# Performance work log

Measured on AMD Instinct MI355X. Metric: run time of the kernel, lower is better.

## Reference

```python
import jax, jax.numpy as jnp
import numpy as np

H = 16       # num heads
D = 128      # head_dim
R = 64       # d_rope_latent
HID = 2048   # hidden_size
DL = 512     # d_latent
EPS = 1e-6


def _rmsnorm(x, g):
    return x * jax.lax.rsqrt(jnp.mean(x * x, axis=-1, keepdims=True) + EPS) * g


def setup_inputs() -> dict:
    key = jax.random.key(0)
    ks = jax.random.split(key, 8)
    B, S = 2, 2048
    s = 0.02
    return {
        "x":   jax.random.normal(ks[0], (B, S, HID), jnp.float32),
        "Wq":  jax.random.normal(ks[1], (HID, H * D), jnp.float32) * s,
        "Wkv": jax.random.normal(ks[2], (HID, DL), jnp.float32) * s,
        "Wkr": jax.random.normal(ks[3], (DL, H * R), jnp.float32) * s,
        "Wkn": jax.random.normal(ks[4], (DL, H * (D - R)), jnp.float32) * s,
        "Wv":  jax.random.normal(ks[5], (DL, H * D), jnp.float32) * s,
        "Wo":  jax.random.normal(ks[6], (H * D, HID), jnp.float32) * s,
        "gq":  jnp.ones((D,), jnp.float32),
        "gk":  jnp.ones((D,), jnp.float32),
    }


def reference(x, Wq, Wkv, Wkr, Wkn, Wv, Wo, gq, gk):
    B, S, _ = x.shape
    # q projection + per-head RMSNorm
    q = _rmsnorm((x @ Wq).reshape(B, S, H, D), gq)          # [B,S,H,D]
    # low-rank KV latent
    lat = x @ Wkv                                            # [B,S,DL]
    kr = (lat @ Wkr).reshape(B, S, H, R)                     # rope part
    kn = (lat @ Wkn).reshape(B, S, H, D - R)                 # nope part
    # pos_encoding is None in source -> no rotation applied, just concat
    k = _rmsnorm(jnp.concatenate([kr, kn], axis=-1), gk)     # [B,S,H,D]
    v = (lat @ Wv).reshape(B, S, H, D)
    # causal SDPA
    scale = 1.0 / jnp.sqrt(jnp.float32(D))
    scores = jnp.einsum('bqhd,bkhd->bhqk', q, k) * scale     # [B,H,S,S]
    causal = jnp.tril(jnp.ones((S, S), bool))
    scores = jnp.where(causal, scores, jnp.float32(-1e30))
    p = jax.nn.softmax(scores, axis=-1)
    o = jnp.einsum('bhqk,bkhd->bqhd', p, v).reshape(B, S, H * D)
    return o @ Wo
```

## Files before the change

kernel.cpp:

```cpp
#include <hip/hip_runtime.h>
#include <cstdint>
#include <cstddef>

typedef short v8s __attribute__((ext_vector_type(8)));
typedef float v4f __attribute__((ext_vector_type(4)));

__device__ inline float bs2f(short s) {
    return __uint_as_float(((unsigned int)(unsigned short)s) << 16);
}
__device__ inline short f2bs(float f) {
    unsigned int u = __float_as_uint(f);
    unsigned int r = (u + 0x7fffu + ((u >> 16) & 1u)) >> 16;
    return (short)r;
}

#define MFMA(a, b, c) __builtin_amdgcn_mfma_f32_16x16x32_bf16((a), (b), (c), 0, 0, 0)

#define GLOAD_LDS16(g, l)                                                  \
    __builtin_amdgcn_global_load_lds(                                      \
        (const __attribute__((address_space(1))) void*)(g),                \
        (__attribute__((address_space(3))) void*)(l), 16, 0, 0)

__global__ __launch_bounds__(256) void prep(const float* __restrict__ x,
                                            short* __restrict__ xb,
                                            const float* __restrict__ Wq,
                                            const float* __restrict__ Wkv,
                                            const float* __restrict__ Wkr,
                                            const float* __restrict__ Wkn,
                                            const float* __restrict__ Wv,
                                            const float* __restrict__ Wo,
                                            short* __restrict__ WtA,
                                            short* __restrict__ WtB,
                                            short* __restrict__ Wot) {
    int blk = blockIdx.x;
    if (blk < 8192) {
        int i = (blk * 256 + threadIdx.x) * 4;
        float4 v = *(const float4*)(x + i);
        short r[4] = {f2bs(v.x), f2bs(v.y), f2bs(v.z), f2bs(v.w)};
        *(uint2*)(xb + i) = *(const uint2*)r;
        return;
    }
    blk -= 8192;
    const float* W;
    short* Wt;
    int K, N, bx, by;
    if (blk < 4096)      { W = Wq;  Wt = WtA;                      K = 2048; N = 2048; bx = blk & 63; by = blk >> 6; }
    else if (blk < 5120) { blk -= 4096; W = Wkv; Wt = WtA + (size_t)2048 * 2048; K = 2048; N = 512;  bx = blk & 15; by = blk >> 4; }
    else if (blk < 5632) { blk -= 5120; W = Wkr; Wt = WtB;                       K = 512;  N = 1024; bx = blk & 31; by = blk >> 5; }
    else if (blk < 6144) { blk -= 5632; W = Wkn; Wt = WtB + (size_t)1024 * 512;  K = 512;  N = 1024; bx = blk & 31; by = blk >> 5; }
    else if (blk < 7168) { blk -= 6144; W = Wv;  Wt = WtB + (size_t)2048 * 512;  K = 512;  N = 2048; bx = blk & 63; by = blk >> 6; }
    else                 { blk -= 7168; W = Wo;  Wt = Wot;                       K = 2048; N = 2048; bx = blk & 63; by = blk >> 6; }

    __shared__ float tile[32][33];
    const int tx = threadIdx.x & 31, ty = threadIdx.x >> 5;
    const int n0 = bx * 32, k0 = by * 32;
#pragma unroll
    for (int i = 0; i < 32; i += 8) tile[ty + i][tx] = W[(size_t)(k0 + ty + i) * N + n0 + tx];
    __syncthreads();
#pragma unroll
    for (int i = 0; i < 32; i += 8)
        Wt[(size_t)(n0 + ty + i) * K + k0 + tx] = f2bs(tile[tx][ty + i]);
}

__global__ __launch_bounds__(256) void gemm_bt(const short* __restrict__ A,
                                               const short* __restrict__ Bt,
                                               void* __restrict__ C0,
                                               void* __restrict__ C1,
                                               void* __restrict__ C2,
                                               int M, int N, int K, int mode,
                                               const float* __restrict__ g,
                                               float scale) {
    __shared__ short As[128 * 32];
    __shared__ short Bs[128 * 32];
    const int tid = threadIdx.x;
    const int lane = tid & 63, wave = tid >> 6;
    const int l16 = lane & 15, quad = lane >> 4;
    const int wm = (wave >> 1) * 64, wn = (wave & 1) * 64;

    const int gx = gridDim.x;
    const int nwg = gx * gridDim.y;
    const int wg = blockIdx.y * gx + blockIdx.x;
    const int cpx = nwg >> 3;
    const int swz = (wg & 7) * cpx + (wg >> 3);
    const int m0 = (swz / gx) * 128, n0 = (swz % gx) * 128;

    const v4f VZ = {0.f, 0.f, 0.f, 0.f};
    v4f acc[4][4];
#pragma unroll
    for (int i = 0; i < 4; i++)
#pragma unroll
        for (int j = 0; j < 4; j++) acc[i][j] = VZ;

    const int r0 = wave * 32 + (lane >> 2);
    const int r1 = r0 + 16;
    const int c0 = ((lane & 3) ^ ((r0 >> 1) & 3)) * 8;
    const int c1 = ((lane & 3) ^ ((r1 >> 1) & 3)) * 8;
    const short* aSrc0 = A + (size_t)(m0 + r0) * K + c0;
    const short* aSrc1 = A + (size_t)(m0 + r1) * K + c1;
    const short* bSrc0 = Bt + (size_t)(n0 + r0) * K + c0;
    const short* bSrc1 = Bt + (size_t)(n0 + r1) * K + c1;
    short* const ldsA0 = &As[(wave * 32) * 32];
    short* const ldsA1 = &As[(wave * 32 + 16) * 32];
    short* const ldsB0 = &Bs[(wave * 32) * 32];
    short* const ldsB1 = &Bs[(wave * 32 + 16) * 32];

    for (int kk = 0; kk < K; kk += 32) {
        __syncthreads();
        GLOAD_LDS16(aSrc0 + kk, ldsA0);
        GLOAD_LDS16(aSrc1 + kk, ldsA1);
        GLOAD_LDS16(bSrc0 + kk, ldsB0);
        GLOAD_LDS16(bSrc1 + kk, ldsB1);
        __syncthreads();

        v8s af[4], bfr[4];
#pragma unroll
        for (int t = 0; t < 4; t++) {
            const int ra = wm + t * 16 + l16;
            af[t] = *(const v8s*)(&As[ra * 32 + ((quad ^ ((ra >> 1) & 3)) * 8)]);
        }
#pragma unroll
        for (int t = 0; t < 4; t++) {
            const int rb = wn + t * 16 + l16;
            bfr[t] = *(const v8s*)(&Bs[rb * 32 + ((quad ^ ((rb >> 1) & 3)) * 8)]);
        }
#pragma unroll
        for (int i = 0; i < 4; i++)
#pragma unroll
            for (int j = 0; j < 4; j++) acc[i][j] = MFMA(af[i], bfr[j], acc[i][j]);
    }

    if (mode == 2) {
        if (n0 < 2048) {
            __syncthreads();
            float* red = (float*)As;
#pragma unroll
            for (int i = 0; i < 4; i++) {
#pragma unroll
                for (int r = 0; r < 4; r++) {
                    float ss2 = 0.f;
#pragma unroll
                    for (int j = 0; j < 4; j++) { float v = acc[i][j][r]; ss2 += v * v; }
#pragma unroll
                    for (int off2 = 1; off2 < 16; off2 <<= 1) ss2 += __shfl_xor(ss2, off2);
                    if (l16 == 0) red[(wm + i * 16 + quad * 4 + r) * 2 + (wn >> 6)] = ss2;
                }
            }
            __syncthreads();
            float gv[4];
#pragma unroll
            for (int j = 0; j < 4; j++) gv[j] = g[wn + j * 16 + l16];
#pragma unroll
            for (int i = 0; i < 4; i++) {
#pragma unroll
                for (int r = 0; r < 4; r++) {
                    const int rl = wm + i * 16 + quad * 4 + r;
                    const float rs =
                        rsqrtf((red[rl * 2] + red[rl * 2 + 1]) * (1.f / 128.f) + 1e-6f) * scale;
#pragma unroll
                    for (int j = 0; j < 4; j++)
                        ((short*)C0)[(size_t)(m0 + rl) * 2048 + n0 + wn + j * 16 + l16] =
                            f2bs(acc[i][j][r] * rs * gv[j]);
                }
            }
        } else {
#pragma unroll
            for (int i = 0; i < 4; i++)
#pragma unroll
                for (int r = 0; r < 4; r++) {
                    const int row = m0 + wm + i * 16 + quad * 4 + r;
#pragma unroll
                    for (int j = 0; j < 4; j++)
                        ((short*)C1)[(size_t)row * 512 + n0 - 2048 + wn + j * 16 + l16] =
                            f2bs(acc[i][j][r]);
                }
        }
        return;
    }

    if (mode == 3 && n0 >= 2048) {
        short* C = (short*)C2;
#pragma unroll
        for (int i = 0; i < 4; i++) {
            const int row = m0 + wm + i * 16 + quad * 4;
            const int bq = row >> 11, s = row & 2047;
            const int kt = s >> 6, key = s & 63;
#pragma unroll
            for (int j = 0; j < 4; j++) {
                const int col = n0 - 2048 + wn + j * 16 + l16;
                const int hh = col >> 7, d = col & 127;
                size_t base = ((size_t)((bq * 16 + hh) * 32 + kt) * 128 + d) * 64 + key;
                short pk[4];
#pragma unroll
                for (int r = 0; r < 4; r++) pk[r] = f2bs(acc[i][j][r]);
                *(uint2*)(C + base) = *(const uint2*)pk;
            }
        }
        return;
    }

    void* Cb = C0;
    int ld = N, coff = 0;
    if (mode == 3) {
        if (n0 < 1024) { Cb = C0; ld = 1024; coff = 0; }
        else           { Cb = C1; ld = 1024; coff = 1024; }
    }
#pragma unroll
    for (int i = 0; i < 4; i++) {
#pragma unroll
        for (int r = 0; r < 4; r++) {
            const int row = m0 + wm + i * 16 + quad * 4 + r;
#pragma unroll
            for (int j = 0; j < 4; j++) {
                const int col = n0 - coff + wn + j * 16 + l16;
                float v = acc[i][j][r];
                if (mode == 1) ((float*)Cb)[(size_t)row * ld + col] = v;
                else ((short*)Cb)[(size_t)row * ld + col] = f2bs(v);
            }
        }
    }
}

__global__ __launch_bounds__(256) void rmsnorm_k(const short* __restrict__ KR,
                                                 const short* __restrict__ KN,
                                                 const float* __restrict__ g,
                                                 short* __restrict__ Y) {
    const int tid = threadIdx.x;
    const int rh = blockIdx.x * 32 + (tid >> 3);
    const int j = tid & 7;
    const size_t ibase = (size_t)blockIdx.x * 2048 + (size_t)tid * 8;
    v8s a = *(const v8s*)(KR + ibase);
    v8s c = *(const v8s*)(KN + ibase);
    float af[8], cf[8];
    float ss = 0.f;
#pragma unroll
    for (int t = 0; t < 8; t++) {
        af[t] = bs2f(a[t]);
        cf[t] = bs2f(c[t]);
        ss += af[t] * af[t] + cf[t] * cf[t];
    }
#pragma unroll
    for (int off = 1; off < 8; off <<= 1) ss += __shfl_xor(ss, off);
    const float rs = rsqrtf(ss * (1.f / 128.f) + 1e-6f);
    const int m = rh >> 4, h = rh & 15;
    const int b = m >> 11, s = m & 2047;
    const size_t obase = ((size_t)((b * 16 + h) * 32 + (s >> 6)) * 64 + (s & 63)) * 128;
    const float* gp = g + j * 8;
    v8s o0, o1;
#pragma unroll
    for (int t = 0; t < 8; t++) {
        o0[t] = f2bs(af[t] * rs * gp[t]);
        o1[t] = f2bs(cf[t] * rs * gp[64 + t]);
    }
    *(v8s*)(Y + obase + j * 8) = o0;
    *(v8s*)(Y + obase + 64 + j * 8) = o1;
}

#define PSTR 72

__global__ __launch_bounds__(256) void flash_attn(const short* __restrict__ Q,
                                                  const short* __restrict__ Kp,
                                                  const short* __restrict__ Vp,
                                                  short* __restrict__ O, int S) {
    __shared__ short Ks[64 * 128];
    __shared__ short Vs[128 * 64];
    __shared__ short Ps[4][16 * PSTR];

    const int lane = threadIdx.x & 63, w = threadIdx.x >> 6;
    const int l16 = lane & 15, quad = lane >> 4;
    const int blk = blockIdx.x;
    const int g = blk >> 3;
    const int bh = (blk & 7) * 4 + (g & 3);
    const int b = bh >> 4, h = bh & 15;
    const int qb = 31 - (g >> 2);
    const int q0 = qb * 64 + w * 16;

    const int koffE = (lane >> 4) * 128 + (((lane & 15) ^ (lane >> 4)) << 3);
    const int koffO = (lane >> 4) * 128 + (((lane & 15) ^ 4 ^ (lane >> 4)) << 3);
    const int voffc = (lane >> 3) * 64 + (((lane & 7) ^ (lane >> 3)) << 3);
    const int swz = (l16 & 7) * 8;

    v8s bq[4];
    {
        const size_t qbase = ((size_t)(b * S + q0 + l16) * 16 + h) * 128;
#pragma unroll
        for (int kc = 0; kc < 4; kc++)
            bq[kc] = *(const v8s*)(Q + qbase + kc * 32 + quad * 8);
    }

    const v4f VZ = {0.f, 0.f, 0.f, 0.f};
    v4f accO[8];
    v4f accL = VZ;
#pragma unroll
    for (int d = 0; d < 8; d++) accO[d] = VZ;

    const short o1 = 0x3F80;
    const v8s vones = {o1, o1, o1, o1, o1, o1, o1, o1};

    const short* const kbh = Kp + (size_t)(bh * 32) * 8192;
    const short* const vbh = Vp + (size_t)(bh * 32) * 8192;

    const int nkt = qb + 1;
    for (int kt = 0; kt < nkt; ++kt) {
        __syncthreads();
        {
            const short* kb = kbh + (size_t)kt * 8192;
            const short* vb = vbh + (size_t)kt * 8192;
            const int c0 = w * 4;
            GLOAD_LDS16(kb + (c0 + 0) * 512 + koffE, Ks + (c0 + 0) * 512);
            GLOAD_LDS16(kb + (c0 + 1) * 512 + koffO, Ks + (c0 + 1) * 512);
            GLOAD_LDS16(kb + (c0 + 2) * 512 + koffE, Ks + (c0 + 2) * 512);
            GLOAD_LDS16(kb + (c0 + 3) * 512 + koffO, Ks + (c0 + 3) * 512);
            GLOAD_LDS16(vb + (c0 + 0) * 512 + voffc, Vs + (c0 + 0) * 512);
            GLOAD_LDS16(vb + (c0 + 1) * 512 + voffc, Vs + (c0 + 1) * 512);
            GLOAD_LDS16(vb + (c0 + 2) * 512 + voffc, Vs + (c0 + 2) * 512);
            GLOAD_LDS16(vb + (c0 + 3) * 512 + voffc, Vs + (c0 + 3) * 512);
        }
        __syncthreads();

        v4f sc[4];
#pragma unroll
        for (int nt = 0; nt < 4; nt++) {
            v8s ak[4];
            const int krow = (nt * 16 + l16) * 128;
#pragma unroll
            for (int kc = 0; kc < 4; kc++)
                ak[kc] = *(const v8s*)(Ks + krow + ((quad * 8 + kc * 32) ^ swz));
            v4f s = VZ;
#pragma unroll
            for (int kc = 0; kc < 4; kc++) s = MFMA(ak[kc], bq[kc], s);
            sc[nt] = s;
        }

        if (kt == nkt - 1) {
            const int qrow = q0 + l16;
            const int k0 = kt * 64;
#pragma unroll
            for (int nt = 0; nt < 4; nt++)
#pragma unroll
                for (int r = 0; r < 4; r++)
                    if (k0 + nt * 16 + quad * 4 + r > qrow) sc[nt][r] = -1e30f;
        }

#pragma unroll
        for (int nt = 0; nt < 4; nt++) {
            short pk[4];
#pragma unroll
            for (int r = 0; r < 4; r++) {
                float p = exp2f(sc[nt][r] - 20.f);
                pk[r] = (short)(__float_as_uint(p) >> 16);
            }
            *(uint2*)(&Ps[w][l16 * PSTR + nt * 16 + quad * 4]) = *(const uint2*)pk;
        }

        v8s ap[2];
#pragma unroll
        for (int kc2 = 0; kc2 < 2; kc2++)
            ap[kc2] = *(const v8s*)(&Ps[w][l16 * PSTR + kc2 * 32 + quad * 8]);
#pragma unroll
        for (int dt = 0; dt < 8; dt++) {
            const int vrow = (dt * 16 + l16) * 64;
#pragma unroll
            for (int kc2 = 0; kc2 < 2; kc2++) {
                v8s bv = *(const v8s*)(Vs + vrow + ((quad * 8 + kc2 * 32) ^ swz));
                accO[dt] = MFMA(ap[kc2], bv, accO[dt]);
            }
        }
#pragma unroll
        for (int kc2 = 0; kc2 < 2; kc2++) accL = MFMA(ap[kc2], vones, accL);
    }

#pragma unroll
    for (int r = 0; r < 4; r++) {
        const int rl = quad * 4 + r;
        const int qg = q0 + rl;
        const float inv = 1.f / accL[r];
        const size_t obase = ((size_t)(b * S + qg) * 16 + h) * 128;
#pragma unroll
        for (int dt = 0; dt < 8; dt++)
            O[obase + dt * 16 + l16] = f2bs(accO[dt][r] * inv);
    }
}

extern "C" void kernel_launch(void* const* d_in, const int* in_sizes, int n_in,
                              void* d_out, int out_size, void* d_ws, size_t ws_size,
                              hipStream_t stream) {
    (void)in_sizes; (void)n_in; (void)out_size; (void)ws_size;
    const float* x   = (const float*)d_in[0];
    const float* Wq  = (const float*)d_in[1];
    const float* Wkv = (const float*)d_in[2];
    const float* Wkr = (const float*)d_in[3];
    const float* Wkn = (const float*)d_in[4];
    const float* Wv  = (const float*)d_in[5];
    const float* Wo  = (const float*)d_in[6];
    const float* gq  = (const float*)d_in[7];
    const float* gk  = (const float*)d_in[8];

    const int B = 2, S = 2048, HID = 2048;
    const int M = B * S;

    char* ws = (char*)d_ws;
    size_t off = 0;
    auto alloc = [&](size_t bytes) {
        char* p = ws + off;
        off += (bytes + 255) & ~(size_t)255;
        return p;
    };
    short* xb   = (short*)alloc((size_t)M * HID * 2);
    short* WtA  = (short*)alloc((size_t)2560 * 2048 * 2);
    short* WtB  = (short*)alloc((size_t)4096 * 512 * 2);
    short* Wot  = (short*)alloc((size_t)2048 * 2048 * 2);
    short* qb   = (short*)alloc((size_t)M * 2048 * 2);
    short* lat  = (short*)alloc((size_t)M * 512 * 2);
    short* krr  = (short*)alloc((size_t)M * 1024 * 2);
    short* knr  = (short*)alloc((size_t)M * 1024 * 2);
    short* Kp   = (short*)alloc((size_t)M * 2048 * 2);
    short* Vp   = (short*)alloc((size_t)M * 2048 * 2);
    short* ob   = (short*)alloc((size_t)M * 2048 * 2);

    prep<<<19456, 256, 0, stream>>>(x, xb, Wq, Wkv, Wkr, Wkn, Wv, Wo, WtA, WtB, Wot);

    gemm_bt<<<dim3(2560 / 128, M / 128), 256, 0, stream>>>(
        xb, WtA, qb, lat, nullptr, M, 2560, 2048, 2, gq,
        0.08838834764831845f * 1.4426950408889634f);

    gemm_bt<<<dim3(4096 / 128, M / 128), 256, 0, stream>>>(
        lat, WtB, krr, knr, Vp, M, 4096, 512, 3, nullptr, 0.f);
    rmsnorm_k<<<(M * 16) / 32, 256, 0, stream>>>(krr, knr, gk, Kp);

    flash_attn<<<dim3(1024), 256, 0, stream>>>(qb, Kp, Vp, ob, S);

    gemm_bt<<<dim3(2048 / 128, M / 128), 256, 0, stream>>>(
        ob, Wot, d_out, nullptr, nullptr, M, 2048, 2048, 1, nullptr, 0.f);
}
```

Measured before the change: 355.0 us.

## Process two 64-row query sub-blocks per flash-attention block to reuse K/V tiles

Each attention block now handles 128 query rows (two sub-tiles of 16 rows per wave) instead of 64, so every K/V tile loaded into LDS is used by twice as many MFMAs and the grid is halved. The causal mask is now applied on every key tile rather than only the last, and s_setprio hints are added around the MFMA sections. This cuts global/LDS K/V traffic per unit of work but doubles accumulator registers, which may lower occupancy. With 512 blocks, causal load imbalance between blocks also becomes coarser.

```diff
diff --git a/kernel.cpp b/kernel.cpp
--- a/kernel.cpp
+++ b/kernel.cpp
@@ -263,7 +263,7 @@
                                                   short* __restrict__ O, int S) {
     __shared__ short Ks[64 * 128];
     __shared__ short Vs[128 * 64];
-    __shared__ short Ps[4][16 * PSTR];
+    __shared__ short Ps[4][32 * PSTR];
 
     const int lane = threadIdx.x & 63, w = threadIdx.x >> 6;
     const int l16 = lane & 15, quad = lane >> 4;
@@ -271,27 +271,33 @@
     const int g = blk >> 3;
     const int bh = (blk & 7) * 4 + (g & 3);
     const int b = bh >> 4, h = bh & 15;
-    const int qb = 31 - (g >> 2);
-    const int q0 = qb * 64 + w * 16;
+    const int qb = 15 - (g >> 2);
+    const int q0 = qb * 128;
 
     const int koffE = (lane >> 4) * 128 + (((lane & 15) ^ (lane >> 4)) << 3);
     const int koffO = (lane >> 4) * 128 + (((lane & 15) ^ 4 ^ (lane >> 4)) << 3);
     const int voffc = (lane >> 3) * 64 + (((lane & 7) ^ (lane >> 3)) << 3);
     const int swz = (l16 & 7) * 8;
 
-    v8s bq[4];
-    {
-        const size_t qbase = ((size_t)(b * S + q0 + l16) * 16 + h) * 128;
+    v8s bq[2][4];
+#pragma unroll
+    for (int s = 0; s < 2; s++) {
+        const size_t qbase =
+            ((size_t)(b * S + q0 + s * 64 + w * 16 + l16) * 16 + h) * 128;
 #pragma unroll
         for (int kc = 0; kc < 4; kc++)
-            bq[kc] = *(const v8s*)(Q + qbase + kc * 32 + quad * 8);
+            bq[s][kc] = *(const v8s*)(Q + qbase + kc * 32 + quad * 8);
     }
 
     const v4f VZ = {0.f, 0.f, 0.f, 0.f};
-    v4f accO[8];
-    v4f accL = VZ;
-#pragma unroll
-    for (int d = 0; d < 8; d++) accO[d] = VZ;
+    v4f accO[2][8];
+    v4f accL[2];
+#pragma unroll
+    for (int s = 0; s < 2; s++) {
+        accL[s] = VZ;
+#pragma unroll
+        for (int d = 0; d < 8; d++) accO[s][d] = VZ;
+    }
 
     const short o1 = 0x3F80;
     const v8s vones = {o1, o1, o1, o1, o1, o1, o1, o1};
@@ -299,7 +305,7 @@
     const short* const kbh = Kp + (size_t)(bh * 32) * 8192;
     const short* const vbh = Vp + (size_t)(bh * 32) * 8192;
 
-    const int nkt = qb + 1;
+    const int nkt = 2 * qb + 2;
     for (int kt = 0; kt < nkt; ++kt) {
         __syncthreads();
         {
@@ -317,7 +323,8 @@
         }
         __syncthreads();
 
-        v4f sc[4];
+        v4f sc[2][4];
+        __builtin_amdgcn_s_setprio(1);
 #pragma unroll
         for (int nt = 0; nt < 4; nt++) {
             v8s ak[4];
@@ -325,60 +332,80 @@
 #pragma unroll
             for (int kc = 0; kc < 4; kc++)
                 ak[kc] = *(const v8s*)(Ks + krow + ((quad * 8 + kc * 32) ^ swz));
-            v4f s = VZ;
-#pragma unroll
-            for (int kc = 0; kc < 4; kc++) s = MFMA(ak[kc], bq[kc], s);
-            sc[nt] = s;
-        }
-
-        if (kt == nkt - 1) {
-            const int qrow = q0 + l16;
-            const int k0 = kt * 64;
+            v4f s0 = VZ, s1 = VZ;
+#pragma unroll
+            for (int kc = 0; kc < 4; kc++) {
+                s0 = MFMA(ak[kc], bq[0][kc], s0);
+                s1 = MFMA(ak[kc], bq[1][kc], s1);
+            }
+            sc[0][nt] = s0;
+            sc[1][nt] = s1;
+        }
+        __builtin_amdgcn_s_setprio(0);
+
+        const int k0 = kt * 64;
+#pragma unroll
+        for (int s = 0; s < 2; s++) {
+            const int qrow = q0 + s * 64 + w * 16 + l16;
 #pragma unroll
             for (int nt = 0; nt < 4; nt++)
 #pragma unroll
                 for (int r = 0; r < 4; r++)
-                    if (k0 + nt * 16 + quad * 4 + r > qrow) sc[nt][r] = -1e30f;
-        }
-
-#pragma unroll
-        for (int nt = 0; nt < 4; nt++) {
-            short pk[4];
-#pragma unroll
-            for (int r = 0; r < 4; r++) {
-                float p = exp2f(sc[nt][r] - 20.f);
-                pk[r] = (short)(__float_as_uint(p) >> 16);
-            }
-            *(uint2*)(&Ps[w][l16 * PSTR + nt * 16 + quad * 4]) = *(const uint2*)pk;
-        }
-
-        v8s ap[2];
-#pragma unroll
-        for (int kc2 = 0; kc2 < 2; kc2++)
-            ap[kc2] = *(const v8s*)(&Ps[w][l16 * PSTR + kc2 * 32 + quad * 8]);
+                    if (k0 + nt * 16 + quad * 4 + r > qrow) sc[s][nt][r] = -1e30f;
+        }
+
+#pragma unroll
+        for (int s = 0; s < 2; s++)
+#pragma unroll
+            for (int nt = 0; nt < 4; nt++) {
+                short pk[4];
+#pragma unroll
+                for (int r = 0; r < 4; r++) {
+                    float p = exp2f(sc[s][nt][r] - 20.f);
+                    pk[r] = (short)(__float_as_uint(p) >> 16);
+                }
+                *(uint2*)(&Ps[w][(s * 16 + l16) * PSTR + nt * 16 + quad * 4]) =
+                    *(const uint2*)pk;
+            }
+
+        v8s ap[2][2];
+#pragma unroll
+        for (int s = 0; s < 2; s++)
+#pragma unroll
+            for (int kc2 = 0; kc2 < 2; kc2++)
+                ap[s][kc2] =
+                    *(const v8s*)(&Ps[w][(s * 16 + l16) * PSTR + kc2 * 32 + quad * 8]);
+        __builtin_amdgcn_s_setprio(1);
 #pragma unroll
         for (int dt = 0; dt < 8; dt++) {
             const int vrow = (dt * 16 + l16) * 64;
 #pragma unroll
             for (int kc2 = 0; kc2 < 2; kc2++) {
                 v8s bv = *(const v8s*)(Vs + vrow + ((quad * 8 + kc2 * 32) ^ swz));
-                accO[dt] = MFMA(ap[kc2], bv, accO[dt]);
-            }
-        }
-#pragma unroll
-        for (int kc2 = 0; kc2 < 2; kc2++) accL = MFMA(ap[kc2], vones, accL);
-    }
-
-#pragma unroll
-    for (int r = 0; r < 4; r++) {
-        const int rl = quad * 4 + r;
-        const int qg = q0 + rl;
-        const float inv = 1.f / accL[r];
-        const size_t obase = ((size_t)(b * S + qg) * 16 + h) * 128;
-#pragma unroll
-        for (int dt = 0; dt < 8; dt++)
-            O[obase + dt * 16 + l16] = f2bs(accO[dt][r] * inv);
-    }
+                accO[0][dt] = MFMA(ap[0][kc2], bv, accO[0][dt]);
+                accO[1][dt] = MFMA(ap[1][kc2], bv, accO[1][dt]);
+            }
+        }
+#pragma unroll
+        for (int s = 0; s < 2; s++)
+#pragma unroll
+            for (int kc2 = 0; kc2 < 2; kc2++)
+                accL[s] = MFMA(ap[s][kc2], vones, accL[s]);
+        __builtin_amdgcn_s_setprio(0);
+    }
+
+#pragma unroll
+    for (int s = 0; s < 2; s++)
+#pragma unroll
+        for (int r = 0; r < 4; r++) {
+            const int rl = quad * 4 + r;
+            const int qg = q0 + s * 64 + w * 16 + rl;
+            const float inv = 1.f / accL[s][r];
+            const size_t obase = ((size_t)(b * S + qg) * 16 + h) * 128;
+#pragma unroll
+            for (int dt = 0; dt < 8; dt++)
+                O[obase + dt * 16 + l16] = f2bs(accO[s][dt][r] * inv);
+        }
 }
 
 extern "C" void kernel_launch(void* const* d_in, const int* in_sizes, int n_in,
@@ -427,7 +454,7 @@
         lat, WtB, krr, knr, Vp, M, 4096, 512, 3, nullptr, 0.f);
     rmsnorm_k<<<(M * 16) / 32, 256, 0, stream>>>(krr, knr, gk, Kp);
 
-    flash_attn<<<dim3(1024), 256, 0, stream>>>(qb, Kp, Vp, ob, S);
+    flash_attn<<<dim3(512), 256, 0, stream>>>(qb, Kp, Vp, ob, S);
 
     gemm_bt<<<dim3(2048 / 128, M / 128), 256, 0, stream>>>(
         ob, Wot, d_out, nullptr, nullptr, M, 2048, 2048, 1, nullptr, 0.f);
```

New measurement: 372.0 us. +4.8%, slower.
